# Optimization experiments

Measured on AMD Instinct MI355X. Metric: run time of the kernel, lower is better.

## Reference

```python
import math
import jax, jax.numpy as jnp
import numpy as np

H = 12
D_MODEL = 768
D_K = D_MODEL // H
B, S = 2, 2048


def setup_inputs() -> dict:
    key = jax.random.key(0)
    ks = jax.random.split(key, 12)
    sc = 0.02
    inp = {
        "query": jax.random.normal(ks[0], (B, S, D_MODEL), jnp.float32),
        "key": jax.random.normal(ks[1], (B, S, D_MODEL), jnp.float32),
        "value": jax.random.normal(ks[2], (B, S, D_MODEL), jnp.float32),
        # causal mask [B, S, S]: 1 where attendable
        "mask": jnp.broadcast_to(jnp.tril(jnp.ones((S, S), jnp.int32)), (B, S, S)),
        "Wq": sc * jax.random.normal(ks[3], (D_MODEL, D_MODEL), jnp.float32),
        "bq": jnp.zeros((D_MODEL,), jnp.float32),
        "Wk": sc * jax.random.normal(ks[4], (D_MODEL, D_MODEL), jnp.float32),
        "bk": jnp.zeros((D_MODEL,), jnp.float32),
        "Wv": sc * jax.random.normal(ks[5], (D_MODEL, D_MODEL), jnp.float32),
        "bv": jnp.zeros((D_MODEL,), jnp.float32),
        "Wo": sc * jax.random.normal(ks[6], (D_MODEL, D_MODEL), jnp.float32),
        "bo": jnp.zeros((D_MODEL,), jnp.float32),
    }
    return inp


def reference(query, key, value, mask, Wq, bq, Wk, bk, Wv, bv, Wo, bo):
    b, s, _ = query.shape
    # linear projections (torch Linear: x @ W.T + b), split into heads
    def proj(x, W, bias):
        return (x @ W.T + bias).reshape(b, s, H, D_K).transpose(0, 2, 1, 3)  # [B,H,S,Dk]

    q = proj(query, Wq, bq)
    k = proj(key, Wk, bk)
    v = proj(value, Wv, bv)

    scores = jnp.einsum("bhqd,bhkd->bhqk", q, k) / math.sqrt(D_K)  # [B,H,S,S]
    # exponential time-decay bias over key positions 1..S, shape [1,1,1,S]
    time = jnp.exp(-jnp.arange(1, s + 1, dtype=scores.dtype))[None, None, None, :]
    scores = jnp.where(mask[:, None, :, :] == 0, jnp.asarray(-1e9, scores.dtype), scores)
    p_attn = jax.nn.softmax(scores - time, axis=-1)
    x = jnp.einsum("bhqk,bhkd->bhqd", p_attn, v)  # [B,H,S,Dk]
    x = x.transpose(0, 2, 1, 3).reshape(b, s, H * D_K)
    return x @ Wo.T + bo
```

## Files before the change

kernel.cpp:

```cpp
#include <hip/hip_runtime.h>
#include <hip/hip_bf16.h>
#include <math.h>

typedef __bf16 bf16;
typedef __attribute__((ext_vector_type(8))) __bf16 bf16x8;
typedef __attribute__((ext_vector_type(4))) __bf16 bf16x4;
typedef __attribute__((ext_vector_type(4))) float floatx4;
typedef __attribute__((ext_vector_type(16))) float floatx16;

#define NH 12
#define DK 64
#define DM 768
#define NB 2
#define SEQ 2048
#define MTOT (NB * SEQ)
#define WELEM (DM * DM)
#define XELEM (MTOT * DM)

#define QSCALE 0.1803368801111832f
#define LOG2E 1.4426950408889634f

static __device__ __forceinline__ bf16x8 load8(const bf16* p) {
    return *(const bf16x8*)p;
}
static __device__ __forceinline__ float4 ld4(const float* p) {
    return *(const float4*)p;
}
static __device__ __forceinline__ bf16x8 cvt8(const float4 a, const float4 b) {
    bf16x8 r;
    r[0] = (bf16)a.x; r[1] = (bf16)a.y; r[2] = (bf16)a.z; r[3] = (bf16)a.w;
    r[4] = (bf16)b.x; r[5] = (bf16)b.y; r[6] = (bf16)b.z; r[7] = (bf16)b.w;
    return r;
}
static __device__ __forceinline__ float fast_exp2(float x) {
#if __has_builtin(__builtin_amdgcn_exp2f)
    return __builtin_amdgcn_exp2f(x);
#else
    return __expf(x * 0.6931471805599453f);
#endif
}
static __device__ __forceinline__ floatx16 zero16() {
    floatx16 z;
#pragma unroll
    for (int i = 0; i < 16; i++) z[i] = 0.f;
    return z;
}
static __device__ __forceinline__ void async16(const bf16* g, bf16* l) {
    __builtin_amdgcn_global_load_lds((const __attribute__((address_space(1))) void*)g,
                                     (__attribute__((address_space(3))) void*)l,
                                     16, 0, 0);
}

__global__ __launch_bounds__(256) void cvt_kernel(
    const float* __restrict__ wq, const float* __restrict__ wk,
    const float* __restrict__ wv, const float* __restrict__ wo,
    const float* __restrict__ xq, const float* __restrict__ xk, const float* __restrict__ xv,
    bf16* __restrict__ Wb, bf16* __restrict__ Wob,
    bf16* __restrict__ Xqb, bf16* __restrict__ Xkb, bf16* __restrict__ Xvb) {
    const int g = blockIdx.x * 256 + threadIdx.x;
    const int PW = WELEM / 8;
    const int PX = XELEM / 8;
    if (g < 4 * PW) {
        const int wi = g / PW;
        const int rem = g - wi * PW;
        const int n = rem / 96;
        const int t = rem - n * 96;
        const int s = t >> 3;
        const int j = t & 7;
        const float* src = (wi == 0) ? wq : (wi == 1) ? wk : (wi == 2) ? wv : wo;
        bf16* dst = (wi < 3) ? (Wb + (size_t)wi * WELEM) : Wob;
        const float* p = src + (size_t)n * DM + s * 64 + j * 8;
        *(bf16x8*)(dst + (size_t)n * DM + s * 64 + ((j ^ (n & 7)) * 8)) = cvt8(ld4(p), ld4(p + 4));
    } else {
        const int gx = g - 4 * PW;
        const int xi = gx / PX;
        const int rem = gx - xi * PX;
        const int m = rem / 96;
        const int t = rem - m * 96;
        const int s = t >> 3;
        const int j = t & 7;
        const float* src = (xi == 0) ? xq : (xi == 1) ? xk : xv;
        bf16* dst = (xi == 0) ? Xqb : (xi == 1) ? Xkb : Xvb;
        const float* p = src + (size_t)m * DM + s * 64 + j * 8;
        *(bf16x8*)(dst + (size_t)m * DM + s * 64 + ((j ^ (m & 7)) * 8)) = cvt8(ld4(p), ld4(p + 4));
    }
}

__global__ __launch_bounds__(256, 3) void qkv_kernel(
    const bf16* __restrict__ Xqb, const bf16* __restrict__ Xkb, const bf16* __restrict__ Xvb,
    const bf16* __restrict__ Wb,
    const float* __restrict__ bq, const float* __restrict__ bk, const float* __restrict__ bv,
    bf16* __restrict__ Oq, bf16* __restrict__ Ok, bf16* __restrict__ Ov) {
    __shared__ __align__(16) bf16 SM[2 * 64 * 64 + 2 * 128 * 64];
    bf16* As0 = SM;
    bf16* Bs0 = SM + 8192;

    const int tid = threadIdx.x;
    const int id = blockIdx.x;
    const int xcd = id & 7;
    const int sl = id >> 3;
    const int z = sl / 48;
    const int r = sl % 48;
    const int m0 = (xcd * 8 + r / 6) * 64;
    const int n0 = (r % 6) * 128;

    const bf16* X = (z == 0) ? Xqb : (z == 1) ? Xkb : Xvb;
    const bf16* W = Wb + (size_t)z * WELEM;
    const float* bias = (z == 0) ? bq : (z == 1) ? bk : bv;
    bf16* out = (z == 0) ? Oq : (z == 1) ? Ok : Ov;

    const int wv = tid >> 6;
    const int wm = wv >> 1, wn = wv & 1;
    const int lane = tid & 63;
    const int ln = lane & 15;
    const int kq = lane >> 4;
    const int drow = lane >> 3;
    const int dcol = (lane & 7) * 8;

    floatx4 acc[2][4];
#pragma unroll
    for (int i = 0; i < 2; i++)
#pragma unroll
        for (int j = 0; j < 4; j++) acc[i][j] = (floatx4){0.f, 0.f, 0.f, 0.f};

#pragma unroll
    for (int it = 0; it < 2; it++)
        async16(X + (size_t)(m0 + wv * 16 + it * 8 + drow) * DM + dcol,
                As0 + (wv * 16 + it * 8) * 64);
#pragma unroll
    for (int it = 0; it < 4; it++)
        async16(W + (size_t)(n0 + wv * 32 + it * 8 + drow) * DM + dcol,
                Bs0 + (wv * 32 + it * 8) * 64);

    for (int k = 0; k < 12; k++) {
        __syncthreads();
        const bf16* Ap = As0 + (k & 1) * 4096;
        const bf16* Bp = Bs0 + (k & 1) * 8192;
        if (k < 11) {
            const int kc = (k + 1) * 64;
            bf16* An = As0 + ((k + 1) & 1) * 4096;
            bf16* Bn = Bs0 + ((k + 1) & 1) * 8192;
#pragma unroll
            for (int it = 0; it < 2; it++)
                async16(X + (size_t)(m0 + wv * 16 + it * 8 + drow) * DM + kc + dcol,
                        An + (wv * 16 + it * 8) * 64);
#pragma unroll
            for (int it = 0; it < 4; it++)
                async16(W + (size_t)(n0 + wv * 32 + it * 8 + drow) * DM + kc + dcol,
                        Bn + (wv * 32 + it * 8) * 64);
        }
#pragma unroll
        for (int ks = 0; ks < 2; ks++) {
            const int jb = (ks * 4 + kq) ^ (ln & 7);
            bf16x8 af[2], bfm[4];
#pragma unroll
            for (int mt = 0; mt < 2; mt++)
                af[mt] = *(const bf16x8*)&Ap[(wm * 32 + mt * 16 + ln) * 64 + jb * 8];
#pragma unroll
            for (int nt = 0; nt < 4; nt++)
                bfm[nt] = *(const bf16x8*)&Bp[(wn * 64 + nt * 16 + ln) * 64 + jb * 8];
#pragma unroll
            for (int mt = 0; mt < 2; mt++)
#pragma unroll
                for (int nt = 0; nt < 4; nt++)
                    acc[mt][nt] = __builtin_amdgcn_mfma_f32_16x16x32_bf16(af[mt], bfm[nt], acc[mt][nt], 0, 0, 0);
        }
    }

    float bv4[4];
#pragma unroll
    for (int nt = 0; nt < 4; nt++) bv4[nt] = bias[n0 + wn * 64 + nt * 16 + ln];

    if (z < 2) {
        const float qs = (z == 0) ? QSCALE : 1.0f;
        __syncthreads();
        bf16 (*E)[136] = (bf16(*)[136])SM;
#pragma unroll
        for (int mt = 0; mt < 2; mt++)
#pragma unroll
            for (int nt = 0; nt < 4; nt++)
#pragma unroll
                for (int r2 = 0; r2 < 4; r2++)
                    E[wm * 32 + mt * 16 + kq * 4 + r2][wn * 64 + nt * 16 + ln] =
                        (bf16)((acc[mt][nt][r2] + bv4[nt]) * qs);
        __syncthreads();
        const int row = tid >> 2;
        const int cb = (tid & 3) * 32;
        const int m = m0 + row;
        const int b = m >> 11;
        const int s = m & (SEQ - 1);
        const int h = (n0 + cb) >> 6;
        const int d = (n0 + cb) & 63;
        bf16* op = &out[((size_t)(b * NH + h) * SEQ + s) * DK + d];
#pragma unroll
        for (int q2 = 0; q2 < 4; q2++)
            *(bf16x8*)(op + q2 * 8) = *(bf16x8*)&E[row][cb + q2 * 8];
    } else {
        __syncthreads();
        bf16 (*E)[72] = (bf16(*)[72])SM;
#pragma unroll
        for (int nt = 0; nt < 4; nt++)
#pragma unroll
            for (int mt = 0; mt < 2; mt++) {
                bf16x4 v;
#pragma unroll
                for (int r2 = 0; r2 < 4; r2++) v[r2] = (bf16)(acc[mt][nt][r2] + bv4[nt]);
                *(bf16x4*)&E[wn * 64 + nt * 16 + ln][wm * 32 + mt * 16 + kq * 4] = v;
            }
        __syncthreads();
        const int row = tid >> 1;
        const int sc = (tid & 1) * 32;
        const int b = m0 >> 11;
        const int s0 = m0 & (SEQ - 1);
        const int h = (n0 >> 6) + (row >> 6);
        const int d = row & 63;
        bf16* op = &out[(size_t)(b * NH + h) * DK * SEQ + (size_t)d * SEQ + s0 + sc];
#pragma unroll
        for (int q2 = 0; q2 < 4; q2++)
            *(bf16x8*)(op + q2 * 8) = *(bf16x8*)&E[row][sc + q2 * 8];
    }
}


#define PERMK(r) (((r) & ~12) | (((r) & 4) << 1) | (((r) & 8) >> 1))
#define VSWZ(g, d) (((g) & 8) | (((g) & 7) ^ ((d) & 7)))

#define STAGE(kc, bfsel)                                                            \
    {                                                                               \
        bf16* kb_ = SM + (bfsel) * 16384;                                           \
        bf16* vb_ = kb_ + 8192;                                                     \
        const int kk0 = (kc) * 128;                                                 \
        _Pragma("unroll")                                                           \
        for (int it = 0; it < 4; it++) {                                            \
            const int sk = wv * 4 + it;                                             \
            const int rK = sk * 8 + (lane >> 3);                                    \
            const int jbK = lane & 7;                                               \
            async16(Kb + (size_t)(kk0 + PERMK(rK)) * DK + ((jbK ^ (rK & 7)) * 8),   \
                    kb_ + sk * 512);                                                \
            const int dV = sk * 4 + (lane >> 4);                                    \
            const int jbV = lane & 15;                                              \
            async16(Vb + (size_t)dV * SEQ + kk0 + (VSWZ(jbV, dV) * 8),              \
                    vb_ + sk * 512);                                                \
        }                                                                           \
    }

#define CHUNK_BODY(FIRSTC)                                                          \
    _Pragma("unroll")                                                               \
    for (int c2 = 0; c2 < 4; c2++) {                                                \
        const int rowk = c2 * 32 + ln32;                                            \
        const bf16* krow = Kc + rowk * 64;                                          \
        const int rs = rowk & 7;                                                    \
        const bf16x8 a0 = *(const bf16x8*)&krow[((0 + hi) ^ rs) * 8];               \
        const bf16x8 a1 = *(const bf16x8*)&krow[((2 + hi) ^ rs) * 8];               \
        const bf16x8 a2 = *(const bf16x8*)&krow[((4 + hi) ^ rs) * 8];               \
        const bf16x8 a3 = *(const bf16x8*)&krow[((6 + hi) ^ rs) * 8];               \
        floatx16 tA = zero16(), tB = zero16();                                      \
        __builtin_amdgcn_s_setprio(1);                                              \
        tA = __builtin_amdgcn_mfma_f32_32x32x16_bf16(a0, qb0, tA, 0, 0, 0);         \
        tA = __builtin_amdgcn_mfma_f32_32x32x16_bf16(a1, qb1, tA, 0, 0, 0);         \
        tB = __builtin_amdgcn_mfma_f32_32x32x16_bf16(a2, qb2, tB, 0, 0, 0);         \
        tB = __builtin_amdgcn_mfma_f32_32x32x16_bf16(a3, qb3, tB, 0, 0, 0);         \
        __builtin_amdgcn_s_setprio(0);                                              \
        bf16x8 pa0, pa1;                                                            \
        _Pragma("unroll")                                                           \
        for (int r = 0; r < 16; r++) {                                              \
            const int kg = k0 + c2 * 32 + ((r >> 3) << 4) + (hi << 3) + (r & 7);    \
            float sv = tA[r] + tB[r];                                               \
            if (FIRSTC) sv -= __expf(-(float)(kg + 1)) * LOG2E;                     \
            float pf = fast_exp2(sv);                                               \
            if (lastc && kg > qgl) pf = 0.f;                                        \
            lsum += pf;                                                             \
            if (r < 8) pa0[r] = (bf16)pf; else pa1[r & 7] = (bf16)pf;               \
        }                                                                           \
        __builtin_amdgcn_s_setprio(1);                                              \
        {                                                                           \
            const bf16* v0 = Vc + ln32 * 128;                                       \
            const bf16* v1 = Vc + (32 + ln32) * 128;                                \
            const int ds = ln32 & 7;                                                \
            bf16x8 vb;                                                              \
            vb = *(const bf16x8*)&v0[VSWZ(c2 * 4 + hi, ds) * 8];                    \
            Oacc0 = __builtin_amdgcn_mfma_f32_32x32x16_bf16(pa0, vb, Oacc0, 0, 0, 0); \
            vb = *(const bf16x8*)&v0[VSWZ(c2 * 4 + 2 + hi, ds) * 8];                \
            Oacc0 = __builtin_amdgcn_mfma_f32_32x32x16_bf16(pa1, vb, Oacc0, 0, 0, 0); \
            vb = *(const bf16x8*)&v1[VSWZ(c2 * 4 + hi, ds) * 8];                    \
            Oacc1 = __builtin_amdgcn_mfma_f32_32x32x16_bf16(pa0, vb, Oacc1, 0, 0, 0); \
            vb = *(const bf16x8*)&v1[VSWZ(c2 * 4 + 2 + hi, ds) * 8];                \
            Oacc1 = __builtin_amdgcn_mfma_f32_32x32x16_bf16(pa1, vb, Oacc1, 0, 0, 0); \
        }                                                                           \
        __builtin_amdgcn_s_setprio(0);                                              \
    }

__global__ __launch_bounds__(256) void attn_kernel(const bf16* __restrict__ Q,
                                                   const bf16* __restrict__ K,
                                                   const bf16* __restrict__ Vt,
                                                   bf16* __restrict__ Xout) {
    __shared__ __align__(16) bf16 SM[2 * 16384];

    const int tid = threadIdx.x;
    const int wv = tid >> 6;
    const int lane = tid & 63;
    const int ln32 = lane & 31;
    const int hi = lane >> 5;

    const int b0 = blockIdx.x;
    const int t = (b0 < 192) ? (15 - b0 / 24) : ((b0 - 192) / 24);
    const int bh = b0 % 24;

    const int q0 = t * 128;
    const int nch = t + 1;

    const bf16* Qb = Q + (size_t)bh * SEQ * DK;
    const bf16* Kb = K + (size_t)bh * SEQ * DK;
    const bf16* Vb = Vt + (size_t)bh * SEQ * DK;

    const int qrow = q0 + wv * 32 + ln32;
    const int qgl = qrow;

    const bf16x8 qb0 = load8(Qb + (size_t)qrow * DK + 0 + hi * 8);
    const bf16x8 qb1 = load8(Qb + (size_t)qrow * DK + 16 + hi * 8);
    const bf16x8 qb2 = load8(Qb + (size_t)qrow * DK + 32 + hi * 8);
    const bf16x8 qb3 = load8(Qb + (size_t)qrow * DK + 48 + hi * 8);

    float lsum = 0.f;
    floatx16 Oacc0 = zero16(), Oacc1 = zero16();

    STAGE(0, 0)

    for (int c = 0; c < nch; c++) {
        const int k0 = c * 128;
        asm volatile("s_waitcnt vmcnt(0)" ::: "memory");
        __syncthreads();
        if (c + 1 < nch) STAGE(c + 1, (c + 1) & 1)
        const bf16* Kc = SM + (c & 1) * 16384;
        const bf16* Vc = Kc + 8192;
        const bool lastc = (c == nch - 1);
        if (c == 0) {
            CHUNK_BODY(true)
        } else {
            CHUNK_BODY(false)
        }
    }

    lsum += __shfl_xor(lsum, 32, 64);
    const float inv = 1.f / lsum;

    __syncthreads();
    bf16 (*E)[72] = (bf16(*)[72])SM;
#pragma unroll
    for (int r = 0; r < 16; r++) {
        const int rq = (r & 3) + ((r >> 2) << 3) + (hi << 2);
        const float rv = __shfl(inv, rq, 64);
        E[wv * 32 + rq][ln32] = (bf16)(Oacc0[r] * rv);
        E[wv * 32 + rq][32 + ln32] = (bf16)(Oacc1[r] * rv);
    }
    __syncthreads();

    const int b = bh / NH;
    const int h = bh - b * NH;
    const int row = tid >> 1;
    const int colh = (tid & 1) * 32;
    const int q = q0 + row;
    const int key = row & 7;
    bf16* rowp = &Xout[((size_t)(b * SEQ + q)) * DM + h * DK];
#pragma unroll
    for (int s2 = 0; s2 < 4; s2++) {
        const int jb = (tid & 1) * 4 + s2;
        *(bf16x8*)(rowp + ((jb ^ key) * 8)) = *(bf16x8*)&E[row][colh + s2 * 8];
    }
}

__global__ __launch_bounds__(256, 3) void outproj_kernel(const bf16* __restrict__ X,
                                                         const bf16* __restrict__ W,
                                                         const float* __restrict__ bias,
                                                         float* __restrict__ out) {
    __shared__ __align__(16) bf16 SM[2 * 64 * 64 + 2 * 128 * 64];
    bf16* As0 = SM;
    bf16* Bs0 = SM + 8192;

    const int tid = threadIdx.x;
    const int id = blockIdx.x;
    const int xcd = id & 7;
    const int sl = id >> 3;
    const int m0 = (xcd * 8 + sl / 6) * 64;
    const int n0 = (sl % 6) * 128;

    const int wv = tid >> 6;
    const int wm = wv >> 1, wn = wv & 1;
    const int lane = tid & 63;
    const int ln = lane & 15;
    const int kq = lane >> 4;
    const int drow = lane >> 3;
    const int dcol = (lane & 7) * 8;

    floatx4 acc[2][4];
#pragma unroll
    for (int i = 0; i < 2; i++)
#pragma unroll
        for (int j = 0; j < 4; j++) acc[i][j] = (floatx4){0.f, 0.f, 0.f, 0.f};

#pragma unroll
    for (int it = 0; it < 2; it++)
        async16(X + (size_t)(m0 + wv * 16 + it * 8 + drow) * DM + dcol,
                As0 + (wv * 16 + it * 8) * 64);
#pragma unroll
    for (int it = 0; it < 4; it++)
        async16(W + (size_t)(n0 + wv * 32 + it * 8 + drow) * DM + dcol,
                Bs0 + (wv * 32 + it * 8) * 64);

    for (int k = 0; k < 12; k++) {
        __syncthreads();
        const bf16* Ap = As0 + (k & 1) * 4096;
        const bf16* Bp = Bs0 + (k & 1) * 8192;
        if (k < 11) {
            const int kc = (k + 1) * 64;
            bf16* An = As0 + ((k + 1) & 1) * 4096;
            bf16* Bn = Bs0 + ((k + 1) & 1) * 8192;
#pragma unroll
            for (int it = 0; it < 2; it++)
                async16(X + (size_t)(m0 + wv * 16 + it * 8 + drow) * DM + kc + dcol,
                        An + (wv * 16 + it * 8) * 64);
#pragma unroll
            for (int it = 0; it < 4; it++)
                async16(W + (size_t)(n0 + wv * 32 + it * 8 + drow) * DM + kc + dcol,
                        Bn + (wv * 32 + it * 8) * 64);
        }
#pragma unroll
        for (int ks = 0; ks < 2; ks++) {
            const int jb = (ks * 4 + kq) ^ (ln & 7);
            bf16x8 af[2], bfm[4];
#pragma unroll
            for (int mt = 0; mt < 2; mt++)
                af[mt] = *(const bf16x8*)&Ap[(wm * 32 + mt * 16 + ln) * 64 + jb * 8];
#pragma unroll
            for (int nt = 0; nt < 4; nt++)
                bfm[nt] = *(const bf16x8*)&Bp[(wn * 64 + nt * 16 + ln) * 64 + jb * 8];
#pragma unroll
            for (int mt = 0; mt < 2; mt++)
#pragma unroll
                for (int nt = 0; nt < 4; nt++)
                    acc[mt][nt] = __builtin_amdgcn_mfma_f32_16x16x32_bf16(af[mt], bfm[nt], acc[mt][nt], 0, 0, 0);
        }
    }

#pragma unroll
    for (int nt = 0; nt < 4; nt++) {
        const int n = n0 + wn * 64 + nt * 16 + ln;
        const float bval = bias[n];
#pragma unroll
        for (int mt = 0; mt < 2; mt++)
#pragma unroll
            for (int r2 = 0; r2 < 4; r2++) {
                const int m = m0 + wm * 32 + mt * 16 + kq * 4 + r2;
                out[(size_t)m * DM + n] = acc[mt][nt][r2] + bval;
            }
    }
}

extern "C" void kernel_launch(void* const* d_in, const int* in_sizes, int n_in,
                              void* d_out, int out_size, void* d_ws, size_t ws_size,
                              hipStream_t stream) {
    const float* query = (const float*)d_in[0];
    const float* key   = (const float*)d_in[1];
    const float* value = (const float*)d_in[2];
    const float* Wq = (const float*)d_in[4];
    const float* bq = (const float*)d_in[5];
    const float* Wk = (const float*)d_in[6];
    const float* bk = (const float*)d_in[7];
    const float* Wv = (const float*)d_in[8];
    const float* bv = (const float*)d_in[9];
    const float* Wo = (const float*)d_in[10];
    const float* bo = (const float*)d_in[11];
    float* out = (float*)d_out;

    bf16* Qws  = (bf16*)d_ws;
    bf16* Kws  = Qws + XELEM;
    bf16* Vtws = Kws + XELEM;
    bf16* Xws  = Vtws + XELEM;
    bf16* Wob  = Xws + XELEM;
    bf16* Xvb  = Wob + WELEM;

    bf16* Wb  = (bf16*)out;
    bf16* Xkb = (bf16*)out + 3 * WELEM;

    bf16* Xqb = Xws;

    const int ncvt = (4 * (WELEM / 8) + 3 * (XELEM / 8)) / 256;
    cvt_kernel<<<ncvt, 256, 0, stream>>>(Wq, Wk, Wv, Wo, query, key, value,
                                         Wb, Wob, Xqb, Xkb, Xvb);

    qkv_kernel<<<1152, 256, 0, stream>>>(Xqb, Xkb, Xvb, Wb, bq, bk, bv,
                                         Qws, Kws, Vtws);

    attn_kernel<<<384, 256, 0, stream>>>(Qws, Kws, Vtws, Xws);

    outproj_kernel<<<384, 256, 0, stream>>>(Xws, Wob, bo, out);
}
```

Measured before the change: 207.0 us.

## Split attention key chunks across two wave groups per block with LDS reduction

The attention kernel now launches 512 threads per block as two groups of four waves. Each group handles alternate 128-key chunks of the causal range, so a block runs twice as many waves over the same query tile. Partial O accumulators and row sums are combined through LDS at the end. This drops the previous double-buffered prefetch (staging and compute are now serialized within each round), adds a float reduction pass through shared memory, and merges the two split QK accumulators into one dependent MFMA chain.

```diff
diff --git a/kernel.cpp b/kernel.cpp
--- a/kernel.cpp
+++ b/kernel.cpp
@@ -225,14 +225,14 @@
 #define PERMK(r) (((r) & ~12) | (((r) & 4) << 1) | (((r) & 8) >> 1))
 #define VSWZ(g, d) (((g) & 8) | (((g) & 7) ^ ((d) & 7)))
 
-#define STAGE(kc, bfsel)                                                            \
+#define STAGE(kc)                                                                   \
     {                                                                               \
-        bf16* kb_ = SM + (bfsel) * 16384;                                           \
+        bf16* kb_ = SM + group * 16384;                                             \
         bf16* vb_ = kb_ + 8192;                                                     \
         const int kk0 = (kc) * 128;                                                 \
         _Pragma("unroll")                                                           \
         for (int it = 0; it < 4; it++) {                                            \
-            const int sk = wv * 4 + it;                                             \
+            const int sk = qw * 4 + it;                                             \
             const int rK = sk * 8 + (lane >> 3);                                    \
             const int jbK = lane & 7;                                               \
             async16(Kb + (size_t)(kk0 + PERMK(rK)) * DK + ((jbK ^ (rK & 7)) * 8),   \
@@ -254,18 +254,18 @@
         const bf16x8 a1 = *(const bf16x8*)&krow[((2 + hi) ^ rs) * 8];               \
         const bf16x8 a2 = *(const bf16x8*)&krow[((4 + hi) ^ rs) * 8];               \
         const bf16x8 a3 = *(const bf16x8*)&krow[((6 + hi) ^ rs) * 8];               \
-        floatx16 tA = zero16(), tB = zero16();                                      \
+        floatx16 t = zero16();                                                      \
         __builtin_amdgcn_s_setprio(1);                                              \
-        tA = __builtin_amdgcn_mfma_f32_32x32x16_bf16(a0, qb0, tA, 0, 0, 0);         \
-        tA = __builtin_amdgcn_mfma_f32_32x32x16_bf16(a1, qb1, tA, 0, 0, 0);         \
-        tB = __builtin_amdgcn_mfma_f32_32x32x16_bf16(a2, qb2, tB, 0, 0, 0);         \
-        tB = __builtin_amdgcn_mfma_f32_32x32x16_bf16(a3, qb3, tB, 0, 0, 0);         \
+        t = __builtin_amdgcn_mfma_f32_32x32x16_bf16(a0, qb0, t, 0, 0, 0);           \
+        t = __builtin_amdgcn_mfma_f32_32x32x16_bf16(a1, qb1, t, 0, 0, 0);           \
+        t = __builtin_amdgcn_mfma_f32_32x32x16_bf16(a2, qb2, t, 0, 0, 0);           \
+        t = __builtin_amdgcn_mfma_f32_32x32x16_bf16(a3, qb3, t, 0, 0, 0);           \
         __builtin_amdgcn_s_setprio(0);                                              \
         bf16x8 pa0, pa1;                                                            \
         _Pragma("unroll")                                                           \
         for (int r = 0; r < 16; r++) {                                              \
             const int kg = k0 + c2 * 32 + ((r >> 3) << 4) + (hi << 3) + (r & 7);    \
-            float sv = tA[r] + tB[r];                                               \
+            float sv = t[r];                                                        \
             if (FIRSTC) sv -= __expf(-(float)(kg + 1)) * LOG2E;                     \
             float pf = fast_exp2(sv);                                               \
             if (lastc && kg > qgl) pf = 0.f;                                        \
@@ -290,14 +290,16 @@
         __builtin_amdgcn_s_setprio(0);                                              \
     }
 
-__global__ __launch_bounds__(256) void attn_kernel(const bf16* __restrict__ Q,
+__global__ __launch_bounds__(512) void attn_kernel(const bf16* __restrict__ Q,
                                                    const bf16* __restrict__ K,
                                                    const bf16* __restrict__ Vt,
                                                    bf16* __restrict__ Xout) {
     __shared__ __align__(16) bf16 SM[2 * 16384];
 
     const int tid = threadIdx.x;
-    const int wv = tid >> 6;
+    const int gw = tid >> 6;
+    const int group = gw >> 2;
+    const int qw = gw & 3;
     const int lane = tid & 63;
     const int ln32 = lane & 31;
     const int hi = lane >> 5;
@@ -313,7 +315,7 @@
     const bf16* Kb = K + (size_t)bh * SEQ * DK;
     const bf16* Vb = Vt + (size_t)bh * SEQ * DK;
 
-    const int qrow = q0 + wv * 32 + ln32;
+    const int qrow = q0 + qw * 32 + ln32;
     const int qgl = qrow;
 
     const bf16x8 qb0 = load8(Qb + (size_t)qrow * DK + 0 + hi * 8);
@@ -324,48 +326,80 @@
     float lsum = 0.f;
     floatx16 Oacc0 = zero16(), Oacc1 = zero16();
 
-    STAGE(0, 0)
-
-    for (int c = 0; c < nch; c++) {
-        const int k0 = c * 128;
+    const int R = (nch + 1) >> 1;
+    for (int r = 0; r < R; r++) {
+        const int c = 2 * r + group;
+        const bool active = (c < nch);
+        __syncthreads();
+        if (active) STAGE(c)
         asm volatile("s_waitcnt vmcnt(0)" ::: "memory");
         __syncthreads();
-        if (c + 1 < nch) STAGE(c + 1, (c + 1) & 1)
-        const bf16* Kc = SM + (c & 1) * 16384;
-        const bf16* Vc = Kc + 8192;
-        const bool lastc = (c == nch - 1);
-        if (c == 0) {
-            CHUNK_BODY(true)
-        } else {
-            CHUNK_BODY(false)
+        if (active) {
+            const int k0 = c * 128;
+            const bool lastc = (c == nch - 1);
+            const bf16* Kc = SM + group * 16384;
+            const bf16* Vc = Kc + 8192;
+            if (c == 0) {
+                CHUNK_BODY(true)
+            } else {
+                CHUNK_BODY(false)
+            }
         }
     }
 
     lsum += __shfl_xor(lsum, 32, 64);
-    const float inv = 1.f / lsum;
 
     __syncthreads();
+    float* LF = (float*)SM;
+    float* LS = (float*)SM + 128 * 68;
+    if (group == 1) {
+#pragma unroll
+        for (int r = 0; r < 16; r++) {
+            const int rq = (r & 3) + ((r >> 2) << 3) + (hi << 2);
+            LF[(qw * 32 + rq) * 68 + ln32] = Oacc0[r];
+            LF[(qw * 32 + rq) * 68 + 32 + ln32] = Oacc1[r];
+        }
+        if (hi == 0) LS[qw * 32 + ln32] = lsum;
+    }
+    __syncthreads();
+    float inv = 0.f;
+    if (group == 0) {
+        lsum += LS[qw * 32 + ln32];
+#pragma unroll
+        for (int r = 0; r < 16; r++) {
+            const int rq = (r & 3) + ((r >> 2) << 3) + (hi << 2);
+            Oacc0[r] += LF[(qw * 32 + rq) * 68 + ln32];
+            Oacc1[r] += LF[(qw * 32 + rq) * 68 + 32 + ln32];
+        }
+        inv = 1.f / lsum;
+    }
+    __syncthreads();
+
     bf16 (*E)[72] = (bf16(*)[72])SM;
-#pragma unroll
-    for (int r = 0; r < 16; r++) {
-        const int rq = (r & 3) + ((r >> 2) << 3) + (hi << 2);
-        const float rv = __shfl(inv, rq, 64);
-        E[wv * 32 + rq][ln32] = (bf16)(Oacc0[r] * rv);
-        E[wv * 32 + rq][32 + ln32] = (bf16)(Oacc1[r] * rv);
+    if (group == 0) {
+#pragma unroll
+        for (int r = 0; r < 16; r++) {
+            const int rq = (r & 3) + ((r >> 2) << 3) + (hi << 2);
+            const float rv = __shfl(inv, rq, 64);
+            E[qw * 32 + rq][ln32] = (bf16)(Oacc0[r] * rv);
+            E[qw * 32 + rq][32 + ln32] = (bf16)(Oacc1[r] * rv);
+        }
     }
     __syncthreads();
 
-    const int b = bh / NH;
-    const int h = bh - b * NH;
-    const int row = tid >> 1;
-    const int colh = (tid & 1) * 32;
-    const int q = q0 + row;
-    const int key = row & 7;
-    bf16* rowp = &Xout[((size_t)(b * SEQ + q)) * DM + h * DK];
-#pragma unroll
-    for (int s2 = 0; s2 < 4; s2++) {
-        const int jb = (tid & 1) * 4 + s2;
-        *(bf16x8*)(rowp + ((jb ^ key) * 8)) = *(bf16x8*)&E[row][colh + s2 * 8];
+    if (tid < 256) {
+        const int b = bh / NH;
+        const int h = bh - b * NH;
+        const int row = tid >> 1;
+        const int colh = (tid & 1) * 32;
+        const int q = q0 + row;
+        const int key = row & 7;
+        bf16* rowp = &Xout[((size_t)(b * SEQ + q)) * DM + h * DK];
+#pragma unroll
+        for (int s2 = 0; s2 < 4; s2++) {
+            const int jb = (tid & 1) * 4 + s2;
+            *(bf16x8*)(rowp + ((jb ^ key) * 8)) = *(bf16x8*)&E[row][colh + s2 * 8];
+        }
     }
 }
 
@@ -491,7 +525,7 @@
     qkv_kernel<<<1152, 256, 0, stream>>>(Xqb, Xkb, Xvb, Wb, bq, bk, bv,
                                          Qws, Kws, Vtws);
 
-    attn_kernel<<<384, 256, 0, stream>>>(Qws, Kws, Vtws, Xws);
+    attn_kernel<<<384, 512, 0, stream>>>(Qws, Kws, Vtws, Xws);
 
     outproj_kernel<<<384, 256, 0, stream>>>(Xws, Wob, bo, out);
 }
```

Result: faster. 194.9 us (-5.8%).
